# Kernel optimization log

Hardware: AMD Instinct MI355X
Metric: run time of the kernel (lower is better)

Reference implementation:

```python
import jax, jax.numpy as jnp
import numpy as np

MASK_SUB = 1000000.0  # the module subtracts 1e6 from masked scores (not -inf)

def setup_inputs() -> dict:
    key = jax.random.key(0)
    kq, kk, kv = jax.random.split(key, 3)
    B, S, D = 16, 2048, 64
    q = jax.random.normal(kq, (B, S, D), dtype=jnp.float32)
    k = jax.random.normal(kk, (B, S, D), dtype=jnp.float32)
    v = jax.random.normal(kv, (B, S, D), dtype=jnp.float32)
    return {"q": q, "k": k, "v": v}

def reference(q, k, v):
    d_k = k.shape[-1]
    s = k.shape[-2]
    # scores: [b, s_q, s_k]
    scores = jnp.einsum('bqd,bkd->bqk', q, k) / jnp.sqrt(jnp.asarray(d_k, q.dtype))
    # causal mask: strictly-upper-triangular entries get 1e6 subtracted (matches torch.triu diagonal=1)
    causal = jnp.triu(jnp.ones((s, s), dtype=bool), k=1)
    scores = jnp.where(causal[None, :, :], scores - MASK_SUB, scores)
    weights = jax.nn.softmax(scores, axis=-1)
    return jnp.einsum('bqk,bkd->bqd', weights, v)
```

## Files before the change

kernel.cpp:

```cpp
#include <hip/hip_runtime.h>
#include <stdint.h>


typedef __bf16 bf16x8 __attribute__((ext_vector_type(8)));
typedef float f32x4 __attribute__((ext_vector_type(4)));

#define NB 16
#define SL 2048
#define DH 64

__device__ __forceinline__ __bf16 f2bf(float f) {
    uint32_t u = __builtin_bit_cast(uint32_t, f);
    u += 0x7FFFu + ((u >> 16) & 1u);
    uint16_t h = (uint16_t)(u >> 16);
    return __builtin_bit_cast(__bf16, h);
}

__device__ __forceinline__ void load_lds16(const void* g, void* l) {
    __builtin_amdgcn_global_load_lds(
        (const __attribute__((address_space(1))) uint32_t*)g,
        (__attribute__((address_space(3))) uint32_t*)l, 16, 0, 0);
}

__global__ __launch_bounds__(256) void prepass(
        const float* __restrict__ K, const float* __restrict__ V,
        __bf16* __restrict__ Kb, __bf16* __restrict__ Vt) {
    __shared__ float tl[64][68];
    const int b    = blockIdx.x >> 5;
    const int tile = blockIdx.x & 31;
    const int s0   = tile << 6;
    const int t    = threadIdx.x;
    const int r    = t >> 2;
    const int c0   = (t & 3) * 16;

    const float* Kp = K + ((size_t)(b * SL + s0) + r) * DH + c0;
    float4 f0 = ((const float4*)Kp)[0], f1 = ((const float4*)Kp)[1];
    float4 f2 = ((const float4*)Kp)[2], f3 = ((const float4*)Kp)[3];
    bf16x8 w0, w1;
    w0[0]=f2bf(f0.x); w0[1]=f2bf(f0.y); w0[2]=f2bf(f0.z); w0[3]=f2bf(f0.w);
    w0[4]=f2bf(f1.x); w0[5]=f2bf(f1.y); w0[6]=f2bf(f1.z); w0[7]=f2bf(f1.w);
    w1[0]=f2bf(f2.x); w1[1]=f2bf(f2.y); w1[2]=f2bf(f2.z); w1[3]=f2bf(f2.w);
    w1[4]=f2bf(f3.x); w1[5]=f2bf(f3.y); w1[6]=f2bf(f3.z); w1[7]=f2bf(f3.w);
    __bf16* Kbp = Kb + ((size_t)(b * SL + s0) + r) * DH;
    const int j0 = c0 >> 3;
    *(bf16x8*)(Kbp + ((j0       ^ (r & 7)) * 8)) = w0;
    *(bf16x8*)(Kbp + (((j0 + 1) ^ (r & 7)) * 8)) = w1;

    const float* Vp = V + ((size_t)(b * SL + s0) + r) * DH + c0;
    ((float4*)&tl[r][c0])[0] = ((const float4*)Vp)[0];
    ((float4*)&tl[r][c0])[1] = ((const float4*)Vp)[1];
    ((float4*)&tl[r][c0])[2] = ((const float4*)Vp)[2];
    ((float4*)&tl[r][c0])[3] = ((const float4*)Vp)[3];
    __syncthreads();

    __bf16* img = Vt + ((size_t)(b * 32 + tile)) * 4096;
#pragma unroll
    for (int half = 0; half < 2; ++half) {
        const int c = half * 256 + t;
        const int d = c >> 3, slot = c & 7;
        const int jj = slot ^ (d & 7);
        bf16x8 w;
#pragma unroll
        for (int e = 0; e < 8; ++e) w[e] = f2bf(tl[jj * 8 + e][d]);
        *(bf16x8*)(img + c * 8) = w;
    }
}

__global__ __launch_bounds__(256, 4) void attn_fwd(
        const float* __restrict__ Q, const __bf16* __restrict__ Kb,
        const __bf16* __restrict__ Vt, float* __restrict__ part,
        float* __restrict__ lpart) {
    __shared__ __align__(16) __bf16 lK[2][4096];
    __shared__ __align__(16) __bf16 lV[2][4096];
    __shared__ __align__(16) __bf16 lP[4][1024];

    const int bid = blockIdx.x;
    const int b   = bid & 15;
    const int j   = 79 - (bid >> 4);
    int T, c;
    if (j < 8)        { T = j;                 c = 0; }
    else if (j < 24)  { T = 8 + ((j - 8) >> 1);  c = (j - 8) & 1; }
    else if (j < 48)  { int k = j - 24; T = 16 + k / 3; c = k % 3; }
    else              { int k = j - 48; T = 24 + (k >> 2); c = k & 3; }
    const int kt0 = c * 8;
    const int kt1 = min(kt0 + 8, T + 1);

    const int tid  = threadIdx.x;
    const int wave = tid >> 6, lane = tid & 63, quad = lane >> 4, l16 = lane & 15;
    const int xk   = l16 & 7;
    const int qglob = T * 64 + wave * 16 + l16;

    bf16x8 qf[2];
    const float* qp = Q + ((size_t)b * SL + qglob) * DH;
#pragma unroll
    for (int s = 0; s < 2; ++s) {
        float4 a0 = ((const float4*)(qp + s * 32 + quad * 8))[0];
        float4 a1 = ((const float4*)(qp + s * 32 + quad * 8))[1];
        qf[s][0] = f2bf(a0.x * 0.125f); qf[s][1] = f2bf(a0.y * 0.125f);
        qf[s][2] = f2bf(a0.z * 0.125f); qf[s][3] = f2bf(a0.w * 0.125f);
        qf[s][4] = f2bf(a1.x * 0.125f); qf[s][5] = f2bf(a1.y * 0.125f);
        qf[s][6] = f2bf(a1.z * 0.125f); qf[s][7] = f2bf(a1.w * 0.125f);
    }

    bf16x8 ones;
#pragma unroll
    for (int e = 0; e < 8; ++e) ones[e] = __builtin_bit_cast(__bf16, (uint16_t)0x3F80);

    f32x4 acc[4];
#pragma unroll
    for (int t = 0; t < 4; ++t) acc[t] = (f32x4)0.0f;
    f32x4 accl = (f32x4)0.0f;

    const __bf16* Kbase = Kb + (size_t)b * SL * DH;
    const __bf16* Vbase = Vt + (size_t)b * 32 * 4096;
    __bf16* lPw = lP[wave];

    auto stage = [&](int kt2) {
        const int bufi = kt2 & 1;
        const __bf16* Ks = Kbase + (size_t)kt2 * 4096;
        const __bf16* Vs = Vbase + (size_t)kt2 * 4096;
#pragma unroll
        for (int i2 = 0; i2 < 2; ++i2) {
            load_lds16(Ks + (size_t)(i2 * 256 + tid) * 8,
                       &lK[bufi][(i2 * 256 + wave * 64) * 8]);
            load_lds16(Vs + (size_t)(i2 * 256 + tid) * 8,
                       &lV[bufi][(i2 * 256 + wave * 64) * 8]);
        }
    };

    stage(kt0);
    for (int kt = kt0; kt < kt1; ++kt) {
        __syncthreads();
        if (kt + 1 < kt1) stage(kt + 1);
        const __bf16* K_ = lK[kt & 1];
        const __bf16* V_ = lV[kt & 1];

        f32x4 sc[4];
#pragma unroll
        for (int t = 0; t < 4; ++t) sc[t] = (f32x4)0.0f;
#pragma unroll
        for (int s = 0; s < 2; ++s) {
#pragma unroll
            for (int t = 0; t < 4; ++t) {
                bf16x8 kf = *(const bf16x8*)&K_[(t * 16 + l16) * 64 + (((s * 4 + quad) ^ xk) << 3)];
                sc[t] = __builtin_amdgcn_mfma_f32_16x16x32_bf16(kf, qf[s], sc[t], 0, 0, 0);
            }
        }

        if (kt == T) {
            const int kb = kt * 64;
#pragma unroll
            for (int t = 0; t < 4; ++t)
#pragma unroll
                for (int r = 0; r < 4; ++r)
                    if (kb + t * 16 + quad * 4 + r > qglob) sc[t][r] = -1.0e30f;
        }

#pragma unroll
        for (int t = 0; t < 4; ++t) {
            float p0 = __expf(sc[t][0]), p1 = __expf(sc[t][1]);
            float p2 = __expf(sc[t][2]), p3 = __expf(sc[t][3]);
            uint32_t u0 = __builtin_amdgcn_perm(__builtin_bit_cast(uint32_t, p1),
                                               __builtin_bit_cast(uint32_t, p0), 0x07060302u);
            uint32_t u1 = __builtin_amdgcn_perm(__builtin_bit_cast(uint32_t, p3),
                                               __builtin_bit_cast(uint32_t, p2), 0x07060302u);
            const int cw = 2 * t + (quad >> 1);
            uint2 val; val.x = u0; val.y = u1;
            *(uint2*)&lPw[l16 * 64 + ((cw ^ xk) << 3) + ((quad & 1) << 2)] = val;
        }
        asm volatile("" ::: "memory");

        bf16x8 pf0 = *(const bf16x8*)&lPw[l16 * 64 + (((0 + quad) ^ xk) << 3)];
        bf16x8 pf1 = *(const bf16x8*)&lPw[l16 * 64 + (((4 + quad) ^ xk) << 3)];
        accl = __builtin_amdgcn_mfma_f32_16x16x32_bf16(ones, pf0, accl, 0, 0, 0);
        accl = __builtin_amdgcn_mfma_f32_16x16x32_bf16(ones, pf1, accl, 0, 0, 0);

#pragma unroll
        for (int t = 0; t < 4; ++t) {
            bf16x8 vf = *(const bf16x8*)&V_[(t * 16 + l16) * 64 + (((0 + quad) ^ xk) << 3)];
            acc[t] = __builtin_amdgcn_mfma_f32_16x16x32_bf16(vf, pf0, acc[t], 0, 0, 0);
        }
#pragma unroll
        for (int t = 0; t < 4; ++t) {
            bf16x8 vf = *(const bf16x8*)&V_[(t * 16 + l16) * 64 + (((4 + quad) ^ xk) << 3)];
            acc[t] = __builtin_amdgcn_mfma_f32_16x16x32_bf16(vf, pf1, acc[t], 0, 0, 0);
        }
    }

    float* pp = part + ((size_t)(b * SL + qglob) * 4 + c) * DH + quad * 4;
#pragma unroll
    for (int t = 0; t < 4; ++t) {
        float4 o4;
        o4.x = acc[t][0]; o4.y = acc[t][1]; o4.z = acc[t][2]; o4.w = acc[t][3];
        *(float4*)(pp + t * 16) = o4;
    }
    if (quad == 0)
        lpart[(size_t)(b * SL + qglob) * 4 + c] = accl[0];
}

__global__ __launch_bounds__(256) void combine(
        const float* __restrict__ part, const float* __restrict__ lpart,
        float* __restrict__ O) {
    const int tid = threadIdx.x;
    const int r   = blockIdx.x * 16 + (tid >> 4);
    const int d4  = tid & 15;
    const int T   = (r >> 6) & 31;
    const int nch = (T >> 3) + 1;
    float4 s = make_float4(0.f, 0.f, 0.f, 0.f);
    float ls = 0.f;
    for (int c = 0; c < nch; ++c) {
        float4 p = *(const float4*)(part + ((size_t)r * 4 + c) * DH + d4 * 4);
        s.x += p.x; s.y += p.y; s.z += p.z; s.w += p.w;
        ls += lpart[(size_t)r * 4 + c];
    }
    const float inv = 1.0f / ls;
    float4 o; o.x = s.x * inv; o.y = s.y * inv; o.z = s.z * inv; o.w = s.w * inv;
    *(float4*)(O + (size_t)r * DH + d4 * 4) = o;
}

extern "C" void kernel_launch(void* const* d_in, const int* in_sizes, int n_in,
                              void* d_out, int out_size, void* d_ws, size_t ws_size,
                              hipStream_t stream) {
    const float* q = (const float*)d_in[0];
    const float* k = (const float*)d_in[1];
    const float* v = (const float*)d_in[2];
    float* o = (float*)d_out;
    __bf16* Kb   = (__bf16*)d_ws;
    __bf16* Vt   = Kb + (size_t)NB * SL * DH;
    float*  pt   = (float*)((char*)d_ws + (8u << 20));
    float*  lp   = pt + (size_t)NB * SL * 4 * DH;
    hipLaunchKernelGGL(prepass, dim3(NB * 32), dim3(256), 0, stream, k, v, Kb, Vt);
    hipLaunchKernelGGL(attn_fwd, dim3(1280), dim3(256), 0, stream, q, Kb, Vt, pt, lp);
    hipLaunchKernelGGL(combine, dim3(NB * SL / 16), dim3(256), 0, stream, pt, lp, o);
}
```

Before: 100.2 us.

## Switch attention to 32x32 MFMA with 128-query blocks and finer key split

Each block now covers two adjacent 64-row query tiles (128 queries, 32 per wave) and uses 32x32x16 bf16 MFMA instead of 16x16x32, so every staged K/V tile is shared by twice as many queries. Key chunks shrink from 8 to 4 tiles, giving up to 8 partial results per row, and the grid is rebuilt as 1152 blocks with a new triangular index mapping. The row sum is now accumulated with scalar adds plus a cross-half shuffle rather than a ones-matrix MFMA. In exchange it uses more registers (launch bounds lowered to 3 blocks), writes larger partial buffers, makes combine read more chunks, and leaves waves whose tile is fully masked idle during the diagonal chunk.

```diff
diff --git a/kernel.cpp b/kernel.cpp
--- a/kernel.cpp
+++ b/kernel.cpp
@@ -4,10 +4,12 @@
 
 typedef __bf16 bf16x8 __attribute__((ext_vector_type(8)));
 typedef float f32x4 __attribute__((ext_vector_type(4)));
+typedef float f32x16 __attribute__((ext_vector_type(16)));
 
 #define NB 16
 #define SL 2048
 #define DH 64
+#define NCH 8
 
 __device__ __forceinline__ __bf16 f2bf(float f) {
     uint32_t u = __builtin_bit_cast(uint32_t, f);
@@ -66,50 +68,48 @@
     }
 }
 
-__global__ __launch_bounds__(256, 4) void attn_fwd(
+__global__ __launch_bounds__(256, 3) void attn_fwd(
         const float* __restrict__ Q, const __bf16* __restrict__ Kb,
         const __bf16* __restrict__ Vt, float* __restrict__ part,
         float* __restrict__ lpart) {
     __shared__ __align__(16) __bf16 lK[2][4096];
     __shared__ __align__(16) __bf16 lV[2][4096];
-    __shared__ __align__(16) __bf16 lP[4][1024];
+    __shared__ __align__(16) __bf16 lP[4][2048];
 
     const int bid = blockIdx.x;
     const int b   = bid & 15;
-    const int j   = 79 - (bid >> 4);
-    int T, c;
-    if (j < 8)        { T = j;                 c = 0; }
-    else if (j < 24)  { T = 8 + ((j - 8) >> 1);  c = (j - 8) & 1; }
-    else if (j < 48)  { int k = j - 24; T = 16 + k / 3; c = k % 3; }
-    else              { int k = j - 48; T = 24 + (k >> 2); c = k & 3; }
-    const int kt0 = c * 8;
-    const int kt1 = min(kt0 + 8, T + 1);
+    const int jr  = 71 - (bid >> 4);
+    int Kp_ = 0;
+    while ((Kp_ + 1) * (Kp_ + 2) <= jr) ++Kp_;
+    const int d_  = jr - Kp_ * (Kp_ + 1);
+    const int u   = 2 * Kp_ + (d_ & 1);
+    const int c   = d_ >> 1;
+    const int kt0   = c * 4;
+    const int ktmax = min(kt0 + 4, 2 * u + 2);
 
     const int tid  = threadIdx.x;
-    const int wave = tid >> 6, lane = tid & 63, quad = lane >> 4, l16 = lane & 15;
-    const int xk   = l16 & 7;
-    const int qglob = T * 64 + wave * 16 + l16;
-
-    bf16x8 qf[2];
+    const int wave = tid >> 6, lane = tid & 63;
+    const int col  = lane & 31, h = lane >> 5;
+    const int xk   = col & 7;
+    const int Tw   = 2 * u + (wave >> 1);
+    const int qglob = Tw * 64 + (wave & 1) * 32 + col;
+
+    bf16x8 qf[4];
     const float* qp = Q + ((size_t)b * SL + qglob) * DH;
 #pragma unroll
-    for (int s = 0; s < 2; ++s) {
-        float4 a0 = ((const float4*)(qp + s * 32 + quad * 8))[0];
-        float4 a1 = ((const float4*)(qp + s * 32 + quad * 8))[1];
+    for (int s = 0; s < 4; ++s) {
+        const float* base = qp + s * 16 + h * 8;
+        float4 a0 = ((const float4*)base)[0];
+        float4 a1 = ((const float4*)base)[1];
         qf[s][0] = f2bf(a0.x * 0.125f); qf[s][1] = f2bf(a0.y * 0.125f);
         qf[s][2] = f2bf(a0.z * 0.125f); qf[s][3] = f2bf(a0.w * 0.125f);
         qf[s][4] = f2bf(a1.x * 0.125f); qf[s][5] = f2bf(a1.y * 0.125f);
         qf[s][6] = f2bf(a1.z * 0.125f); qf[s][7] = f2bf(a1.w * 0.125f);
     }
 
-    bf16x8 ones;
-#pragma unroll
-    for (int e = 0; e < 8; ++e) ones[e] = __builtin_bit_cast(__bf16, (uint16_t)0x3F80);
-
-    f32x4 acc[4];
-#pragma unroll
-    for (int t = 0; t < 4; ++t) acc[t] = (f32x4)0.0f;
-    f32x4 accl = (f32x4)0.0f;
+    f32x16 acc[2];
+    acc[0] = (f32x16)0.0f; acc[1] = (f32x16)0.0f;
+    float accl = 0.0f;
 
     const __bf16* Kbase = Kb + (size_t)b * SL * DH;
     const __bf16* Vbase = Vt + (size_t)b * 32 * 4096;
@@ -129,73 +129,70 @@
     };
 
     stage(kt0);
-    for (int kt = kt0; kt < kt1; ++kt) {
+    for (int kt = kt0; kt < ktmax; ++kt) {
         __syncthreads();
-        if (kt + 1 < kt1) stage(kt + 1);
+        if (kt + 1 < ktmax) stage(kt + 1);
+        if (kt > Tw) continue;
         const __bf16* K_ = lK[kt & 1];
         const __bf16* V_ = lV[kt & 1];
 
-        f32x4 sc[4];
-#pragma unroll
-        for (int t = 0; t < 4; ++t) sc[t] = (f32x4)0.0f;
-#pragma unroll
-        for (int s = 0; s < 2; ++s) {
-#pragma unroll
-            for (int t = 0; t < 4; ++t) {
-                bf16x8 kf = *(const bf16x8*)&K_[(t * 16 + l16) * 64 + (((s * 4 + quad) ^ xk) << 3)];
-                sc[t] = __builtin_amdgcn_mfma_f32_16x16x32_bf16(kf, qf[s], sc[t], 0, 0, 0);
-            }
-        }
-
-        if (kt == T) {
-            const int kb = kt * 64;
-#pragma unroll
-            for (int t = 0; t < 4; ++t)
-#pragma unroll
-                for (int r = 0; r < 4; ++r)
-                    if (kb + t * 16 + quad * 4 + r > qglob) sc[t][r] = -1.0e30f;
-        }
-
-#pragma unroll
-        for (int t = 0; t < 4; ++t) {
-            float p0 = __expf(sc[t][0]), p1 = __expf(sc[t][1]);
-            float p2 = __expf(sc[t][2]), p3 = __expf(sc[t][3]);
-            uint32_t u0 = __builtin_amdgcn_perm(__builtin_bit_cast(uint32_t, p1),
-                                               __builtin_bit_cast(uint32_t, p0), 0x07060302u);
-            uint32_t u1 = __builtin_amdgcn_perm(__builtin_bit_cast(uint32_t, p3),
-                                               __builtin_bit_cast(uint32_t, p2), 0x07060302u);
-            const int cw = 2 * t + (quad >> 1);
-            uint2 val; val.x = u0; val.y = u1;
-            *(uint2*)&lPw[l16 * 64 + ((cw ^ xk) << 3) + ((quad & 1) << 2)] = val;
+#pragma unroll
+        for (int mt = 0; mt < 2; ++mt) {
+            f32x16 sc = (f32x16)0.0f;
+            const int key = mt * 32 + col;
+#pragma unroll
+            for (int s = 0; s < 4; ++s) {
+                bf16x8 kf = *(const bf16x8*)&K_[key * 64 + (((2 * s + h) ^ xk) << 3)];
+                sc = __builtin_amdgcn_mfma_f32_32x32x16_bf16(kf, qf[s], sc, 0, 0, 0);
+            }
+            if (kt == Tw) {
+                const int kb = kt * 64 + mt * 32 + 4 * h;
+#pragma unroll
+                for (int g = 0; g < 4; ++g)
+#pragma unroll
+                    for (int r = 0; r < 4; ++r)
+                        if (kb + 8 * g + r > qglob) sc[4 * g + r] = -1.0e30f;
+            }
+#pragma unroll
+            for (int g = 0; g < 4; ++g) {
+                float p0 = __expf(sc[4 * g + 0]), p1 = __expf(sc[4 * g + 1]);
+                float p2 = __expf(sc[4 * g + 2]), p3 = __expf(sc[4 * g + 3]);
+                accl += (p0 + p1) + (p2 + p3);
+                uint32_t u0 = __builtin_amdgcn_perm(__builtin_bit_cast(uint32_t, p1),
+                                                   __builtin_bit_cast(uint32_t, p0), 0x07060302u);
+                uint32_t u1 = __builtin_amdgcn_perm(__builtin_bit_cast(uint32_t, p3),
+                                                   __builtin_bit_cast(uint32_t, p2), 0x07060302u);
+                uint2 val; val.x = u0; val.y = u1;
+                *(uint2*)&lPw[(mt * 4 + g) * 256 + col * 8 + 4 * h] = val;
+            }
         }
         asm volatile("" ::: "memory");
 
-        bf16x8 pf0 = *(const bf16x8*)&lPw[l16 * 64 + (((0 + quad) ^ xk) << 3)];
-        bf16x8 pf1 = *(const bf16x8*)&lPw[l16 * 64 + (((4 + quad) ^ xk) << 3)];
-        accl = __builtin_amdgcn_mfma_f32_16x16x32_bf16(ones, pf0, accl, 0, 0, 0);
-        accl = __builtin_amdgcn_mfma_f32_16x16x32_bf16(ones, pf1, accl, 0, 0, 0);
-
-#pragma unroll
-        for (int t = 0; t < 4; ++t) {
-            bf16x8 vf = *(const bf16x8*)&V_[(t * 16 + l16) * 64 + (((0 + quad) ^ xk) << 3)];
-            acc[t] = __builtin_amdgcn_mfma_f32_16x16x32_bf16(vf, pf0, acc[t], 0, 0, 0);
-        }
-#pragma unroll
-        for (int t = 0; t < 4; ++t) {
-            bf16x8 vf = *(const bf16x8*)&V_[(t * 16 + l16) * 64 + (((4 + quad) ^ xk) << 3)];
-            acc[t] = __builtin_amdgcn_mfma_f32_16x16x32_bf16(vf, pf1, acc[t], 0, 0, 0);
-        }
-    }
-
-    float* pp = part + ((size_t)(b * SL + qglob) * 4 + c) * DH + quad * 4;
-#pragma unroll
-    for (int t = 0; t < 4; ++t) {
-        float4 o4;
-        o4.x = acc[t][0]; o4.y = acc[t][1]; o4.z = acc[t][2]; o4.w = acc[t][3];
-        *(float4*)(pp + t * 16) = o4;
-    }
-    if (quad == 0)
-        lpart[(size_t)(b * SL + qglob) * 4 + c] = accl[0];
+#pragma unroll
+        for (int s = 0; s < 4; ++s) {
+            bf16x8 pf = *(const bf16x8*)&lPw[(2 * s + h) * 256 + col * 8];
+#pragma unroll
+            for (int mt = 0; mt < 2; ++mt) {
+                const int dd = mt * 32 + col;
+                bf16x8 vf = *(const bf16x8*)&V_[dd * 64 + (((2 * s + h) ^ xk) << 3)];
+                acc[mt] = __builtin_amdgcn_mfma_f32_32x32x16_bf16(vf, pf, acc[mt], 0, 0, 0);
+            }
+        }
+    }
+
+    float* pp = part + ((size_t)(b * SL + qglob) * NCH + c) * DH;
+#pragma unroll
+    for (int mt = 0; mt < 2; ++mt)
+#pragma unroll
+        for (int g = 0; g < 4; ++g) {
+            float4 o4;
+            o4.x = acc[mt][4 * g + 0]; o4.y = acc[mt][4 * g + 1];
+            o4.z = acc[mt][4 * g + 2]; o4.w = acc[mt][4 * g + 3];
+            *(float4*)(pp + mt * 32 + 8 * g + 4 * h) = o4;
+        }
+    const float lsum = accl + __shfl_xor(accl, 32);
+    if (h == 0)
+        lpart[(size_t)(b * SL + qglob) * NCH + c] = lsum;
 }
 
 __global__ __launch_bounds__(256) void combine(
@@ -205,13 +202,13 @@
     const int r   = blockIdx.x * 16 + (tid >> 4);
     const int d4  = tid & 15;
     const int T   = (r >> 6) & 31;
-    const int nch = (T >> 3) + 1;
+    const int nch = (T + 4) >> 2;
     float4 s = make_float4(0.f, 0.f, 0.f, 0.f);
     float ls = 0.f;
     for (int c = 0; c < nch; ++c) {
-        float4 p = *(const float4*)(part + ((size_t)r * 4 + c) * DH + d4 * 4);
+        float4 p = *(const float4*)(part + ((size_t)r * NCH + c) * DH + d4 * 4);
         s.x += p.x; s.y += p.y; s.z += p.z; s.w += p.w;
-        ls += lpart[(size_t)r * 4 + c];
+        ls += lpart[(size_t)r * NCH + c];
     }
     const float inv = 1.0f / ls;
     float4 o; o.x = s.x * inv; o.y = s.y * inv; o.z = s.z * inv; o.w = s.w * inv;
@@ -225,11 +222,11 @@
     const float* k = (const float*)d_in[1];
     const float* v = (const float*)d_in[2];
     float* o = (float*)d_out;
-    __bf16* Kb   = (__bf16*)d_ws;
-    __bf16* Vt   = Kb + (size_t)NB * SL * DH;
-    float*  pt   = (float*)((char*)d_ws + (8u << 20));
-    float*  lp   = pt + (size_t)NB * SL * 4 * DH;
+    __bf16* Kb = (__bf16*)d_ws;
+    __bf16* Vt = Kb + (size_t)NB * SL * DH;
+    float*  pt = (float*)((char*)d_ws + (8u << 20));
+    float*  lp = pt + (size_t)NB * SL * NCH * DH;
     hipLaunchKernelGGL(prepass, dim3(NB * 32), dim3(256), 0, stream, k, v, Kb, Vt);
-    hipLaunchKernelGGL(attn_fwd, dim3(1280), dim3(256), 0, stream, q, Kb, Vt, pt, lp);
+    hipLaunchKernelGGL(attn_fwd, dim3(NB * 72), dim3(256), 0, stream, q, Kb, Vt, pt, lp);
     hipLaunchKernelGGL(combine, dim3(NB * SL / 16), dim3(256), 0, stream, pt, lp, o);
 }
```

New measurement: 101.9 us. No clear change (+1.7%).
